# Kernel tuning notes

Measured on AMD Instinct MI355X. Metric: run time of the kernel, lower is better.

Reference implementation:

```python
import jax, jax.numpy as jnp
import numpy as np

B, T, C, H = 4, 2048, 1024, 16
D = C // H  # head_dim = 64

def setup_inputs() -> dict:
    key = jax.random.key(0)
    k1, k2, k3 = jax.random.split(key, 3)
    x = jax.random.normal(k1, (B, T, C), dtype=jnp.float32)
    w_qkv = jax.random.normal(k2, (C, 3 * C), dtype=jnp.float32) * (C ** -0.5)
    w_proj = jax.random.normal(k3, (C, C), dtype=jnp.float32) * (C ** -0.5)
    b_proj = jnp.zeros((C,), dtype=jnp.float32)
    return {"x": x, "w_qkv": w_qkv, "w_proj": w_proj, "b_proj": b_proj}

def reference(x, w_qkv, w_proj, b_proj):
    Bx, Tx, Cx = x.shape
    qkv = x @ w_qkv  # [B,T,3C]
    q, k, v = jnp.split(qkv, 3, axis=-1)
    # [B,T,H,D] -> [B,H,T,D]
    q = q.reshape(Bx, Tx, H, D).transpose(0, 2, 1, 3)
    k = k.reshape(Bx, Tx, H, D).transpose(0, 2, 1, 3)
    v = v.reshape(Bx, Tx, H, D).transpose(0, 2, 1, 3)
    scale = 1.0 / np.sqrt(D).astype(np.float32)
    att = jnp.einsum('bhqd,bhkd->bhqk', q, k) * scale  # [B,H,T,T]
    causal = jnp.tril(jnp.ones((Tx, Tx), dtype=bool))
    att = jnp.where(causal, att, -jnp.inf)
    att = jax.nn.softmax(att, axis=-1)
    y = jnp.einsum('bhqk,bhkd->bhqd', att, v)  # [B,H,T,D]
    y = y.transpose(0, 2, 1, 3).reshape(Bx, Tx, Cx)
    return y @ w_proj + b_proj
```

## Files before the change

kernel.cpp:

```cpp
#include <hip/hip_runtime.h>

typedef unsigned short u16;
typedef unsigned int u32;
typedef __attribute__((ext_vector_type(8))) short bf16x8;
typedef __attribute__((ext_vector_type(4))) float f32x4;
typedef __attribute__((ext_vector_type(16))) float f32x16;
typedef __attribute__((ext_vector_type(4))) unsigned short u16x4;

#define MFMA16(a, b, c) __builtin_amdgcn_mfma_f32_16x16x32_bf16((a), (b), (c), 0, 0, 0)
#define MFMA32(a, b, c) __builtin_amdgcn_mfma_f32_32x32x16_bf16((a), (b), (c), 0, 0, 0)

__device__ __forceinline__ u16 f2bf(float f) {
  union { float f; unsigned int i; } v; v.f = f;
  return (u16)((v.i + 0x7FFFu + ((v.i >> 16) & 1u)) >> 16);
}
__device__ __forceinline__ float b2f(u16 u) {
  union { unsigned int i; float f; } v; v.i = ((unsigned int)u) << 16; return v.f;
}
__device__ __forceinline__ float exp2a(float x) {
  float r; asm("v_exp_f32 %0, %1" : "=v"(r) : "v"(x)); return r;
}
__device__ __forceinline__ u32 cvtpk(float lo, float hi) {
  u32 d; asm("v_cvt_pk_bf16_f32 %0, %1, %2" : "=v"(d) : "v"(lo), "v"(hi)); return d;
}
__device__ __forceinline__ void gl2lds16(const u16* g, u16* l) {
  __builtin_amdgcn_global_load_lds(
      (const __attribute__((address_space(1))) void*)g,
      (__attribute__((address_space(3))) void*)l, 16, 0, 0);
}

__global__ __launch_bounds__(256) void k_ingest(const float* __restrict__ src,
                                                u16* __restrict__ dst, int n8) {
  const int i = blockIdx.x * 256 + threadIdx.x;
  if (i >= n8) return;
  const float* s = src + (size_t)i * 8;
  float4 a = *(const float4*)(s);
  float4 b = *(const float4*)(s + 4);
  union { u16 o[8]; int4 v; } u;
  u.o[0] = f2bf(a.x); u.o[1] = f2bf(a.y); u.o[2] = f2bf(a.z); u.o[3] = f2bf(a.w);
  u.o[4] = f2bf(b.x); u.o[5] = f2bf(b.y); u.o[6] = f2bf(b.z); u.o[7] = f2bf(b.w);
  *(int4*)(&dst[(size_t)i * 8]) = u.v;
}

__global__ __launch_bounds__(256) void k_transpose(const float* __restrict__ src,
                                                   u16* __restrict__ dst, int R, int C) {
  __shared__ u16 tile[64][65];
  const int c0 = blockIdx.x * 64, r0 = blockIdx.y * 64;
  const int t = threadIdx.x;
#pragma unroll
  for (int i = 0; i < 16; ++i) {
    int e = i * 256 + t, rr = e >> 6, cc = e & 63;
    tile[rr][cc] = f2bf(src[(size_t)(r0 + rr) * C + c0 + cc]);
  }
  __syncthreads();
#pragma unroll
  for (int i = 0; i < 16; ++i) {
    int e = i * 256 + t, rr = e >> 6, cc = e & 63;
    dst[(size_t)(c0 + rr) * R + r0 + cc] = tile[cc][rr];
  }
}

template <int QKV>
__global__ __launch_bounds__(256) void k_gemm(
    const u16* __restrict__ A, const u16* __restrict__ Bt,
    const float* __restrict__ bias, float* __restrict__ Cf,
    u16* __restrict__ Qb, u16* __restrict__ Kb, u16* __restrict__ VTb,
    int M, int N, int K) {
  __shared__ __attribute__((aligned(16))) u16 As[128 * 32];
  __shared__ __attribute__((aligned(16))) u16 Bs[128 * 32];
  const int bn = blockIdx.x, bm = blockIdx.y;
  const int t = threadIdx.x, lane = t & 63, w = t >> 6;
  const int wr = w >> 1, wc = w & 1;
  const int rh = lane & 15, kg = lane >> 4;
  const int srow = lane >> 2, sk8 = (lane & 3) << 3;

  f32x4 acc[4][4];
#pragma unroll
  for (int mi = 0; mi < 4; ++mi)
#pragma unroll
    for (int ni = 0; ni < 4; ++ni) acc[mi][ni] = (f32x4)0.0f;

  for (int k0 = 0; k0 < K; k0 += 32) {
#pragma unroll
    for (int i = 0; i < 2; ++i) {
      const int r0 = w * 32 + i * 16;
      gl2lds16(&A[(size_t)(bm * 128 + r0 + srow) * K + k0 + sk8], &As[r0 * 32]);
      gl2lds16(&Bt[(size_t)(bn * 128 + r0 + srow) * K + k0 + sk8], &Bs[r0 * 32]);
    }
    asm volatile("s_waitcnt vmcnt(0)" ::: "memory");
    __syncthreads();

    bf16x8 af[4], bfr[4];
#pragma unroll
    for (int mi = 0; mi < 4; ++mi)
      af[mi] = *(const bf16x8*)(&As[(wr * 64 + mi * 16 + rh) * 32 + kg * 8]);
#pragma unroll
    for (int ni = 0; ni < 4; ++ni)
      bfr[ni] = *(const bf16x8*)(&Bs[(wc * 64 + ni * 16 + rh) * 32 + kg * 8]);
    __builtin_amdgcn_s_setprio(1);
#pragma unroll
    for (int mi = 0; mi < 4; ++mi)
#pragma unroll
      for (int ni = 0; ni < 4; ++ni)
        acc[mi][ni] = MFMA16(af[mi], bfr[ni], acc[mi][ni]);
    __builtin_amdgcn_s_setprio(0);
    __syncthreads();
  }

  if (QKV == 0) {
    const int rbase = bm * 128 + wr * 64;
    const int cbase = bn * 128 + wc * 64;
#pragma unroll
    for (int ni = 0; ni < 4; ++ni) {
      const int col = cbase + ni * 16 + rh;
      const float bv = bias ? bias[col] : 0.0f;
#pragma unroll
      for (int mi = 0; mi < 4; ++mi) {
#pragma unroll
        for (int r = 0; r < 4; ++r) {
          int row = rbase + mi * 16 + kg * 4 + r;
          Cf[(size_t)row * N + col] = acc[mi][ni][r] + bv;
        }
      }
    }
  } else {
    const float SCQ = 0.125f * 1.44269504f;
    const int rowbase = bm * 128 + wr * 64;
    const int b = rowbase >> 11;
    const int tb = rowbase & 2047;
    const int cbase = bn * 128 + wc * 64;
    const int role = cbase >> 10;
    const int h = (cbase & 1023) >> 6;
    const int bh = b * 16 + h;
#pragma unroll
    for (int ni = 0; ni < 4; ++ni) {
      const int d = ni * 16 + rh;
#pragma unroll
      for (int mi = 0; mi < 4; ++mi) {
        const int tt = tb + mi * 16 + kg * 4;
        if (role == 2) {
          u16x4 pk;
#pragma unroll
          for (int r = 0; r < 4; ++r) pk[r] = f2bf(acc[mi][ni][r]);
          *(u16x4*)(&VTb[((size_t)bh * 64 + d) * 2048 + tt]) = pk;
        } else {
          u16* dst = (role == 0) ? Qb : Kb;
          const float sc = (role == 0) ? SCQ : 1.0f;
#pragma unroll
          for (int r = 0; r < 4; ++r)
            dst[((size_t)bh * 2048 + tt + r) * 64 + d] = f2bf(acc[mi][ni][r] * sc);
        }
      }
    }
  }
}

__global__ __launch_bounds__(64, 2) void k_attn(const u16* __restrict__ Qb,
                                                const u16* __restrict__ Kb,
                                                const u16* __restrict__ VTb,
                                                u16* __restrict__ Y,
                                                char* __restrict__ part) {
  const int bh = blockIdx.x;
  const int y = (int)blockIdx.y;
  int sb, t0, t1, half = 0;
  bool spl;
  if (y < 32) {
    sb = 31 - (y >> 1);
    half = y & 1;
    const int hl = sb + 1;
    t0 = half * hl;
    t1 = t0 + hl;
    spl = true;
  } else {
    sb = 47 - y;
    t0 = 0;
    t1 = 2 * sb + 2;
    spl = false;
  }
  const int nt = 2 * sb + 2;
  const int lane = threadIdx.x & 63;
  const int q31 = lane & 31, hi = lane >> 5;
  const int qA = sb * 64 + q31;
  const int qBr = sb * 64 + 32 + q31;
  const u16* Qh = Qb + (size_t)bh * 2048 * 64;
  const u16* Kh = Kb + (size_t)bh * 2048 * 64;
  const u16* Vh = VTb + (size_t)bh * 64 * 2048;
  const int b = bh >> 4, h = bh & 15;

  bf16x8 qfA[4], qfB[4];
#pragma unroll
  for (int d = 0; d < 4; ++d) {
    qfA[d] = *(const bf16x8*)(&Qh[(size_t)qA * 64 + d * 16 + hi * 8]);
    qfB[d] = *(const bf16x8*)(&Qh[(size_t)qBr * 64 + d * 16 + hi * 8]);
  }

  f32x16 oA0 = (f32x16)0.0f, oA1 = (f32x16)0.0f;
  f32x16 oB0 = (f32x16)0.0f, oB1 = (f32x16)0.0f;
  float mA = -1e30f, sA = 0.0f, mB = -1e30f, sB = 0.0f;

  for (int tt = t0; tt < t1; ++tt) {
    const int j0 = tt * 32;
    const bool aAct = tt < nt - 1;

    bf16x8 kf[4];
#pragma unroll
    for (int d = 0; d < 4; ++d)
      kf[d] = *(const bf16x8*)(&Kh[(size_t)(j0 + q31) * 64 + d * 16 + hi * 8]);
    const bf16x8 vf0 = *(const bf16x8*)(&Vh[(size_t)q31 * 2048 + j0 + hi * 8]);
    const bf16x8 vf1 = *(const bf16x8*)(&Vh[(size_t)q31 * 2048 + j0 + 16 + hi * 8]);
    const bf16x8 vf2 = *(const bf16x8*)(&Vh[(size_t)(32 + q31) * 2048 + j0 + hi * 8]);
    const bf16x8 vf3 = *(const bf16x8*)(&Vh[(size_t)(32 + q31) * 2048 + j0 + 16 + hi * 8]);

    f32x16 stB = (f32x16)0.0f;
    __builtin_amdgcn_s_setprio(1);
#pragma unroll
    for (int d = 0; d < 4; ++d) stB = MFMA32(kf[d], qfB[d], stB);
    f32x16 stA = (f32x16)0.0f;
    if (aAct) {
#pragma unroll
      for (int d = 0; d < 4; ++d) stA = MFMA32(kf[d], qfA[d], stA);
    }
    __builtin_amdgcn_s_setprio(0);

    if (tt == nt - 2) {
#pragma unroll
      for (int r = 0; r < 16; ++r) {
        const int kcol = (r & 3) + 8 * (r >> 2) + 4 * hi;
        if (kcol > q31) stA[r] = -1e30f;
      }
    }
    if (tt == nt - 1) {
#pragma unroll
      for (int r = 0; r < 16; ++r) {
        const int kcol = (r & 3) + 8 * (r >> 2) + 4 * hi;
        if (kcol > q31) stB[r] = -1e30f;
      }
    }

    union { u32 w4[4]; bf16x8 f; } paA0, paA1, paB0, paB1;
    if (aAct) {
      float mx = fmaxf(
          fmaxf(fmaxf(fmaxf(stA[0], stA[1]), fmaxf(stA[2], stA[3])),
                fmaxf(fmaxf(stA[4], stA[5]), fmaxf(stA[6], stA[7]))),
          fmaxf(fmaxf(fmaxf(stA[8], stA[9]), fmaxf(stA[10], stA[11])),
                fmaxf(fmaxf(stA[12], stA[13]), fmaxf(stA[14], stA[15]))));
      if (__any(mx - mA > 8.0f)) {
        mx = fmaxf(mx, __shfl_xor(mx, 32));
        const float mn = fmaxf(mA, mx);
        const float scf = exp2a(mA - mn);
        mA = mn; sA *= scf; oA0 *= scf; oA1 *= scf;
      }
      float p[16];
#pragma unroll
      for (int r = 0; r < 16; ++r) p[r] = exp2a(stA[r] - mA);
      sA += (((p[0] + p[1]) + (p[2] + p[3])) + ((p[4] + p[5]) + (p[6] + p[7]))) +
            (((p[8] + p[9]) + (p[10] + p[11])) + ((p[12] + p[13]) + (p[14] + p[15])));
      u32 D0 = cvtpk(p[0], p[1]),   D1 = cvtpk(p[2], p[3]);
      u32 D2 = cvtpk(p[4], p[5]),   D3 = cvtpk(p[6], p[7]);
      u32 D4 = cvtpk(p[8], p[9]),   D5 = cvtpk(p[10], p[11]);
      u32 D6 = cvtpk(p[12], p[13]), D7 = cvtpk(p[14], p[15]);
      u32 X0 = __shfl_xor(D0, 32), X1 = __shfl_xor(D1, 32);
      u32 X2 = __shfl_xor(D2, 32), X3 = __shfl_xor(D3, 32);
      u32 X4 = __shfl_xor(D4, 32), X5 = __shfl_xor(D5, 32);
      u32 X6 = __shfl_xor(D6, 32), X7 = __shfl_xor(D7, 32);
      paA0.w4[0] = hi ? X2 : D0; paA0.w4[1] = hi ? X3 : D1;
      paA0.w4[2] = hi ? D2 : X0; paA0.w4[3] = hi ? D3 : X1;
      paA1.w4[0] = hi ? X6 : D4; paA1.w4[1] = hi ? X7 : D5;
      paA1.w4[2] = hi ? D6 : X4; paA1.w4[3] = hi ? D7 : X5;
    }

    {
      float mx = fmaxf(
          fmaxf(fmaxf(fmaxf(stB[0], stB[1]), fmaxf(stB[2], stB[3])),
                fmaxf(fmaxf(stB[4], stB[5]), fmaxf(stB[6], stB[7]))),
          fmaxf(fmaxf(fmaxf(stB[8], stB[9]), fmaxf(stB[10], stB[11])),
                fmaxf(fmaxf(stB[12], stB[13]), fmaxf(stB[14], stB[15]))));
      if (__any(mx - mB > 8.0f)) {
        mx = fmaxf(mx, __shfl_xor(mx, 32));
        const float mn = fmaxf(mB, mx);
        const float scf = exp2a(mB - mn);
        mB = mn; sB *= scf; oB0 *= scf; oB1 *= scf;
      }
      float p[16];
#pragma unroll
      for (int r = 0; r < 16; ++r) p[r] = exp2a(stB[r] - mB);
      sB += (((p[0] + p[1]) + (p[2] + p[3])) + ((p[4] + p[5]) + (p[6] + p[7]))) +
            (((p[8] + p[9]) + (p[10] + p[11])) + ((p[12] + p[13]) + (p[14] + p[15])));
      u32 D0 = cvtpk(p[0], p[1]),   D1 = cvtpk(p[2], p[3]);
      u32 D2 = cvtpk(p[4], p[5]),   D3 = cvtpk(p[6], p[7]);
      u32 D4 = cvtpk(p[8], p[9]),   D5 = cvtpk(p[10], p[11]);
      u32 D6 = cvtpk(p[12], p[13]), D7 = cvtpk(p[14], p[15]);
      u32 X0 = __shfl_xor(D0, 32), X1 = __shfl_xor(D1, 32);
      u32 X2 = __shfl_xor(D2, 32), X3 = __shfl_xor(D3, 32);
      u32 X4 = __shfl_xor(D4, 32), X5 = __shfl_xor(D5, 32);
      u32 X6 = __shfl_xor(D6, 32), X7 = __shfl_xor(D7, 32);
      paB0.w4[0] = hi ? X2 : D0; paB0.w4[1] = hi ? X3 : D1;
      paB0.w4[2] = hi ? D2 : X0; paB0.w4[3] = hi ? D3 : X1;
      paB1.w4[0] = hi ? X6 : D4; paB1.w4[1] = hi ? X7 : D5;
      paB1.w4[2] = hi ? D6 : X4; paB1.w4[3] = hi ? D7 : X5;
    }

    __builtin_amdgcn_s_setprio(1);
    oB0 = MFMA32(vf0, paB0.f, oB0);
    oB0 = MFMA32(vf1, paB1.f, oB0);
    oB1 = MFMA32(vf2, paB0.f, oB1);
    oB1 = MFMA32(vf3, paB1.f, oB1);
    if (aAct) {
      oA0 = MFMA32(vf0, paA0.f, oA0);
      oA0 = MFMA32(vf1, paA1.f, oA0);
      oA1 = MFMA32(vf2, paA0.f, oA1);
      oA1 = MFMA32(vf3, paA1.f, oA1);
    }
    __builtin_amdgcn_s_setprio(0);
  }

  sA += __shfl_xor(sA, 32);
  sB += __shfl_xor(sB, 32);

  if (!spl) {
    const float invA = 1.0f / sA, invB = 1.0f / sB;
    u16* yrowA = Y + ((size_t)b * 2048 + qA) * 1024 + h * 64;
    u16* yrowB = Y + ((size_t)b * 2048 + qBr) * 1024 + h * 64;
#pragma unroll
    for (int a = 0; a < 4; ++a) {
      u16x4 pk;
#pragma unroll
      for (int i = 0; i < 4; ++i) pk[i] = f2bf(oA0[a * 4 + i] * invA);
      *(u16x4*)(yrowA + a * 8 + 4 * hi) = pk;
#pragma unroll
      for (int i = 0; i < 4; ++i) pk[i] = f2bf(oA1[a * 4 + i] * invA);
      *(u16x4*)(yrowA + 32 + a * 8 + 4 * hi) = pk;
#pragma unroll
      for (int i = 0; i < 4; ++i) pk[i] = f2bf(oB0[a * 4 + i] * invB);
      *(u16x4*)(yrowB + a * 8 + 4 * hi) = pk;
#pragma unroll
      for (int i = 0; i < 4; ++i) pk[i] = f2bf(oB1[a * 4 + i] * invB);
      *(u16x4*)(yrowB + 32 + a * 8 + 4 * hi) = pk;
    }
  } else {
    const size_t pbase = ((size_t)(bh * 16 + (sb - 16)) * 2 + half) * 64;
    char* pA = part + (pbase + q31) * 144;
    char* pB = part + (pbase + 32 + q31) * 144;
    if (!hi) {
      ((float*)pA)[0] = mA; ((float*)pA)[1] = sA;
      ((float*)pB)[0] = mB; ((float*)pB)[1] = sB;
    }
    u16* oA = (u16*)(pA + 8);
    u16* oB = (u16*)(pB + 8);
#pragma unroll
    for (int a = 0; a < 4; ++a) {
      u16x4 pk;
#pragma unroll
      for (int i = 0; i < 4; ++i) pk[i] = f2bf(oA0[a * 4 + i]);
      *(u16x4*)(oA + a * 8 + 4 * hi) = pk;
#pragma unroll
      for (int i = 0; i < 4; ++i) pk[i] = f2bf(oA1[a * 4 + i]);
      *(u16x4*)(oA + 32 + a * 8 + 4 * hi) = pk;
#pragma unroll
      for (int i = 0; i < 4; ++i) pk[i] = f2bf(oB0[a * 4 + i]);
      *(u16x4*)(oB + a * 8 + 4 * hi) = pk;
#pragma unroll
      for (int i = 0; i < 4; ++i) pk[i] = f2bf(oB1[a * 4 + i]);
      *(u16x4*)(oB + 32 + a * 8 + 4 * hi) = pk;
    }
  }
}

__global__ __launch_bounds__(256) void k_comb(const char* __restrict__ part,
                                              u16* __restrict__ Y) {
  const int g = blockIdx.x * 4 + (threadIdx.x >> 6);
  const int d = threadIdx.x & 63;
  const int bh = g >> 10, sbi = (g >> 6) & 15, r = g & 63;
  const char* p1 = part + ((size_t)((bh * 16 + sbi) * 2 + 0) * 64 + r) * 144;
  const char* p2 = part + ((size_t)((bh * 16 + sbi) * 2 + 1) * 64 + r) * 144;
  const float m1 = ((const float*)p1)[0], s1 = ((const float*)p1)[1];
  const float m2 = ((const float*)p2)[0], s2 = ((const float*)p2)[1];
  const float mm = fmaxf(m1, m2);
  const float e1 = exp2a(m1 - mm), e2 = exp2a(m2 - mm);
  const float inv = 1.0f / (s1 * e1 + s2 * e2);
  const float o1 = b2f(((const u16*)(p1 + 8))[d]);
  const float o2 = b2f(((const u16*)(p2 + 8))[d]);
  const int b = bh >> 4, h = bh & 15;
  const int row = (16 + sbi) * 64 + r;
  Y[((size_t)b * 2048 + row) * 1024 + h * 64 + d] = f2bf((o1 * e1 + o2 * e2) * inv);
}

extern "C" void kernel_launch(void* const* d_in, const int* in_sizes, int n_in,
                              void* d_out, int out_size, void* d_ws, size_t ws_size,
                              hipStream_t stream) {
  const float* x      = (const float*)d_in[0];
  const float* w_qkv  = (const float*)d_in[1];
  const float* w_proj = (const float*)d_in[2];
  const float* b_proj = (const float*)d_in[3];
  float* out = (float*)d_out;

  char* ws = (char*)d_ws;
  u16* wqkvT  = (u16*)(ws);
  u16* wprojT = (u16*)(ws + 6291456);
  u16* Qb     = (u16*)(ws + 8388608);
  u16* Kb     = (u16*)(ws + 25165824);
  u16* VTb    = (u16*)(ws + 41943040);
  u16* xb     = (u16*)(ws + 58720256);
  u16* Yb     = xb;
  char* part  = (char*)d_out;

  k_ingest<<<4096, 256, 0, stream>>>(x, xb, 1048576);
  k_transpose<<<dim3(48, 16), 256, 0, stream>>>(w_qkv, wqkvT, 1024, 3072);
  k_transpose<<<dim3(16, 16), 256, 0, stream>>>(w_proj, wprojT, 1024, 1024);
  k_gemm<1><<<dim3(24, 64), 256, 0, stream>>>(xb, wqkvT, nullptr, nullptr,
                                              Qb, Kb, VTb, 8192, 3072, 1024);
  k_attn<<<dim3(64, 48), 64, 0, stream>>>(Qb, Kb, VTb, Yb, part);
  k_comb<<<16384, 256, 0, stream>>>(part, Yb);
  k_gemm<0><<<dim3(8, 64), 256, 0, stream>>>(Yb, wprojT, b_proj, out,
                                             nullptr, nullptr, nullptr, 8192, 1024, 1024);
}
```

Measured before the change: 220.7 us.

## Rebalance causal attention work with three-way splits for long query blocks

```diff
diff --git a/kernel.cpp b/kernel.cpp
--- a/kernel.cpp
+++ b/kernel.cpp
@@ -162,20 +162,28 @@
                                                 char* __restrict__ part) {
   const int bh = blockIdx.x;
   const int y = (int)blockIdx.y;
-  int sb, t0, t1, half = 0;
+  int sb, t0, t1, slot = 0;
   bool spl;
-  if (y < 32) {
-    sb = 31 - (y >> 1);
-    half = y & 1;
+  if (y < 12) {
+    sb = y; t0 = 0; t1 = 2 * sb + 2; spl = false;
+  } else if (y < 36) {
+    const int idx = y - 12;
+    sb = 12 + (idx >> 1);
+    const int c = idx & 1;
     const int hl = sb + 1;
-    t0 = half * hl;
-    t1 = t0 + hl;
+    t0 = c * hl; t1 = t0 + hl;
     spl = true;
+    slot = (sb - 12) * 2 + c;
   } else {
-    sb = 47 - y;
-    t0 = 0;
-    t1 = 2 * sb + 2;
-    spl = false;
+    const int idx = y - 36;
+    sb = 24 + idx / 3;
+    const int c = idx - (sb - 24) * 3;
+    const int ntl = 2 * sb + 2;
+    const int base = ntl / 3, rem = ntl % 3;
+    t0 = c * base + (c < rem ? c : rem);
+    t1 = t0 + base + (c < rem ? 1 : 0);
+    spl = true;
+    slot = 24 + (sb - 24) * 3 + c;
   }
   const int nt = 2 * sb + 2;
   const int lane = threadIdx.x & 63;
@@ -338,7 +346,7 @@
       *(u16x4*)(yrowB + 32 + a * 8 + 4 * hi) = pk;
     }
   } else {
-    const size_t pbase = ((size_t)(bh * 16 + (sb - 16)) * 2 + half) * 64;
+    const size_t pbase = ((size_t)bh * 48 + slot) * 64;
     char* pA = part + (pbase + q31) * 144;
     char* pB = part + (pbase + 32 + q31) * 144;
     if (!hi) {
@@ -368,21 +376,32 @@
 
 __global__ __launch_bounds__(256) void k_comb(const char* __restrict__ part,
                                               u16* __restrict__ Y) {
-  const int g = blockIdx.x * 4 + (threadIdx.x >> 6);
+  const int bh = blockIdx.x;
+  const int rr = blockIdx.y * 4 + (threadIdx.x >> 6);
   const int d = threadIdx.x & 63;
-  const int bh = g >> 10, sbi = (g >> 6) & 15, r = g & 63;
-  const char* p1 = part + ((size_t)((bh * 16 + sbi) * 2 + 0) * 64 + r) * 144;
-  const char* p2 = part + ((size_t)((bh * 16 + sbi) * 2 + 1) * 64 + r) * 144;
-  const float m1 = ((const float*)p1)[0], s1 = ((const float*)p1)[1];
-  const float m2 = ((const float*)p2)[0], s2 = ((const float*)p2)[1];
-  const float mm = fmaxf(m1, m2);
-  const float e1 = exp2a(m1 - mm), e2 = exp2a(m2 - mm);
-  const float inv = 1.0f / (s1 * e1 + s2 * e2);
-  const float o1 = b2f(((const u16*)(p1 + 8))[d]);
-  const float o2 = b2f(((const u16*)(p2 + 8))[d]);
+  const int sbi = rr >> 6;
+  const int sb = 12 + sbi;
+  const int r = rr & 63;
+  const int n = (sb < 24) ? 2 : 3;
+  const int slot0 = (sb < 24) ? (sb - 12) * 2 : 24 + (sb - 24) * 3;
+  const char* p[3];
+  float mv[3], sv[3];
+  float mm = -1e30f;
+  for (int i = 0; i < n; ++i) {
+    p[i] = part + (((size_t)bh * 48 + slot0 + i) * 64 + r) * 144;
+    mv[i] = ((const float*)p[i])[0];
+    sv[i] = ((const float*)p[i])[1];
+    mm = fmaxf(mm, mv[i]);
+  }
+  float stot = 0.0f, otot = 0.0f;
+  for (int i = 0; i < n; ++i) {
+    const float e = exp2a(mv[i] - mm);
+    stot += sv[i] * e;
+    otot += b2f(((const u16*)(p[i] + 8))[d]) * e;
+  }
   const int b = bh >> 4, h = bh & 15;
-  const int row = (16 + sbi) * 64 + r;
-  Y[((size_t)b * 2048 + row) * 1024 + h * 64 + d] = f2bf((o1 * e1 + o2 * e2) * inv);
+  const int row = sb * 64 + r;
+  Y[((size_t)b * 2048 + row) * 1024 + h * 64 + d] = f2bf(otot / stot);
 }
 
 extern "C" void kernel_launch(void* const* d_in, const int* in_sizes, int n_in,
@@ -409,8 +428,8 @@
   k_transpose<<<dim3(16, 16), 256, 0, stream>>>(w_proj, wprojT, 1024, 1024);
   k_gemm<1><<<dim3(24, 64), 256, 0, stream>>>(xb, wqkvT, nullptr, nullptr,
                                               Qb, Kb, VTb, 8192, 3072, 1024);
-  k_attn<<<dim3(64, 48), 64, 0, stream>>>(Qb, Kb, VTb, Yb, part);
-  k_comb<<<16384, 256, 0, stream>>>(part, Yb);
+  k_attn<<<dim3(64, 60), 64, 0, stream>>>(Qb, Kb, VTb, Yb, part);
+  k_comb<<<dim3(64, 320), 256, 0, stream>>>(part, Yb);
   k_gemm<0><<<dim3(8, 64), 256, 0, stream>>>(Yb, wprojT, b_proj, out,
                                              nullptr, nullptr, nullptr, 8192, 1024, 1024);
 }
```

New measurement: 232.0 us. 5.1% more time.
